# Optimization experiments

Measured on AMD Instinct MI355X. Metric: run time of the kernel, lower is better.

Reference implementation:

```python
import jax, jax.numpy as jnp
import numpy as np

N, D = 50000, 1000
FH1, FH2 = 256, 128
GH1, GH2, H = 64, 30, 3
NC = 10
E = 800000
BN_EPS = 1e-5


def setup_inputs() -> dict:
    key = jax.random.key(0)
    ks = iter(jax.random.split(key, 48))
    nk = lambda: next(ks)
    r = lambda *s: jax.random.normal(nk(), s, jnp.float32) * 0.05
    g = lambda n: 1.0 + jax.random.normal(nk(), (n,), jnp.float32) * 0.01
    return dict(
        x=jax.random.normal(nk(), (N, D), jnp.float32),
        edge_index=jax.random.randint(nk(), (2, E), 0, N, dtype=jnp.int32),
        enc_w1=r(D, FH1), enc_b1=r(FH1), enc_g1=g(FH1), enc_bt1=r(FH1),
        enc_w2=r(FH1, FH2), enc_b2=r(FH2), enc_g2=g(FH2), enc_bt2=r(FH2),
        gat1_w=r(FH2, H * GH1), gat1_asrc=r(H, GH1), gat1_adst=r(H, GH1), gat1_b=r(H * GH1),
        gat2_w=r(H * GH1, GH2), gat2_asrc=r(1, GH2), gat2_adst=r(1, GH2), gat2_b=r(GH2),
        gat3_w=r(H * GH1, GH2), gat3_asrc=r(1, GH2), gat3_adst=r(1, GH2), gat3_b=r(GH2),
        dec_w1=r(GH2, FH2), dec_b1=r(FH2), dec_g1=g(FH2), dec_bt1=r(FH2),
        dec_w2=r(FH2, FH1), dec_b2=r(FH1), dec_g2=g(FH1), dec_bt2=r(FH1),
        dec_w3=r(FH1, D), dec_b3=r(D),
        clu_w1=r(GH2, FH2), clu_b1=r(FH2), clu_g1=g(FH2), clu_bt1=r(FH2),
        clu_w2=r(FH2, NC), clu_b2=r(NC),
    )


def _bn_elu(h, w, b, gm, bt):
    # Linear -> BatchNorm1d (batch stats) -> ELU; dropout is identity at eval
    h = h @ w + b
    m = h.mean(0)
    v = h.var(0)
    return jax.nn.elu(gm * (h - m) * jax.lax.rsqrt(v + BN_EPS) + bt)


def _gat(h, src, dst, n, w, a_src, a_dst, b, heads, oc, concat):
    # PyG GATConv: per-head linear, edge-wise LeakyReLU(0.2) scores,
    # softmax over incoming edges of each dst node, weighted scatter-sum.
    hh = (h @ w).reshape(n, heads, oc)            # [N,H,C]
    s_src = jnp.sum(hh * a_src, -1)               # [N,H]
    s_dst = jnp.sum(hh * a_dst, -1)               # [N,H]
    e = jax.nn.leaky_relu(s_src[src] + s_dst[dst], negative_slope=0.2)  # [E,H]
    m = jax.ops.segment_max(e, dst, num_segments=n)
    p = jnp.exp(e - m[dst])
    denom = jax.ops.segment_sum(p, dst, num_segments=n)
    alpha = p / denom[dst]                        # [E,H]
    msg = hh[src] * alpha[..., None]              # [E,H,C]
    out = jax.ops.segment_sum(msg, dst, num_segments=n)
    out = out.reshape(n, heads * oc) if concat else out.mean(1)
    return out + b


def reference(x, edge_index,
              enc_w1, enc_b1, enc_g1, enc_bt1, enc_w2, enc_b2, enc_g2, enc_bt2,
              gat1_w, gat1_asrc, gat1_adst, gat1_b,
              gat2_w, gat2_asrc, gat2_adst, gat2_b,
              gat3_w, gat3_asrc, gat3_adst, gat3_b,
              dec_w1, dec_b1, dec_g1, dec_bt1, dec_w2, dec_b2, dec_g2, dec_bt2, dec_w3, dec_b3,
              clu_w1, clu_b1, clu_g1, clu_bt1, clu_w2, clu_b2):
    n = x.shape[0]
    loops = jnp.arange(n, dtype=edge_index.dtype)  # GATConv add_self_loops=True
    src = jnp.concatenate([edge_index[0], loops])
    dst = jnp.concatenate([edge_index[1], loops])

    h = _bn_elu(x, enc_w1, enc_b1, enc_g1, enc_bt1)
    h = _bn_elu(h, enc_w2, enc_b2, enc_g2, enc_bt2)
    h = jax.nn.relu(_gat(h, src, dst, n, gat1_w, gat1_asrc, gat1_adst, gat1_b, H, GH1, True))
    mu = _gat(h, src, dst, n, gat2_w, gat2_asrc, gat2_adst, gat2_b, 1, GH2, False)
    logvar = _gat(h, src, dst, n, gat3_w, gat3_asrc, gat3_adst, gat3_b, 1, GH2, False)
    z = mu  # eval-mode reparameterize returns mu

    d = _bn_elu(z, dec_w1, dec_b1, dec_g1, dec_bt1)
    d = _bn_elu(d, dec_w2, dec_b2, dec_g2, dec_bt2)
    x_rec = d @ dec_w3 + dec_b3

    c = _bn_elu(z, clu_w1, clu_b1, clu_g1, clu_bt1)
    pred = jax.nn.softmax(c @ clu_w2 + clu_b2, axis=1)
    return (pred, x_rec, z, mu, logvar)
```

## Files before the change

### kernel.cpp

```cpp
#include <hip/hip_runtime.h>
#include <hip/hip_bf16.h>

typedef short short8 __attribute__((ext_vector_type(8)));
typedef short short4v __attribute__((ext_vector_type(4)));
typedef float f32x4 __attribute__((ext_vector_type(4)));

static __device__ __forceinline__ short f2bf(float f){
  __hip_bfloat16 h = __float2bfloat16(f);
  return __builtin_bit_cast(short, h);
}
static __device__ __forceinline__ float b2f(short s){
  unsigned int u = ((unsigned int)(unsigned short)s) << 16;
  return __builtin_bit_cast(float, u);
}
static __device__ __forceinline__ float lrelu(float x){ return x > 0.f ? x : 0.2f*x; }
static __device__ __forceinline__ float eluf(float x){ return x > 0.f ? x : (__expf(x)-1.f); }
static __device__ __forceinline__ int imin(int a,int b){ return a<b?a:b; }

typedef const __attribute__((address_space(1))) void as1_void;
typedef __attribute__((address_space(3))) void as3_void;
static __device__ __forceinline__ void gload16(const void* g, void* l){
  __builtin_amdgcn_global_load_lds((as1_void*)g, (as3_void*)l, 16, 0, 0);
}
template<int NN> __device__ __forceinline__ void wait_vm(){
  if constexpr (NN==0) asm volatile("s_waitcnt vmcnt(0)" ::: "memory");
  else if constexpr (NN==3) asm volatile("s_waitcnt vmcnt(3)" ::: "memory");
  else if constexpr (NN==4) asm volatile("s_waitcnt vmcnt(4)" ::: "memory");
  else if constexpr (NN==6) asm volatile("s_waitcnt vmcnt(6)" ::: "memory");
  else if constexpr (NN==8) asm volatile("s_waitcnt vmcnt(8)" ::: "memory");
}

__global__ __launch_bounds__(256) void cvt_x(const float* __restrict__ x, short* __restrict__ xb, int M){
  int row = blockIdx.x*2 + (threadIdx.x>>7);
  int c8  = (threadIdx.x&127)*8;
  if (row >= M || c8 >= 1000) return;
  const float* p = x + (size_t)row*1000 + c8;
  float4 f0 = *(const float4*)p, f1 = *(const float4*)(p+4);
  short8 o;
  o[0]=f2bf(f0.x);o[1]=f2bf(f0.y);o[2]=f2bf(f0.z);o[3]=f2bf(f0.w);
  o[4]=f2bf(f1.x);o[5]=f2bf(f1.y);o[6]=f2bf(f1.z);o[7]=f2bf(f1.w);
  *(short8*)&xb[(size_t)row*1000 + c8] = o;
}

template<int BN, bool OBF16, bool CSTATS>
__global__ __launch_bounds__(256) void gemm_g(
    const short* __restrict__ A, int lda, const short* __restrict__ Bt, int ldb,
    void* __restrict__ Cv, const float* __restrict__ bias,
    float* __restrict__ ssum, float* __restrict__ ssq,
    int M, int N, int K, int ldc)
{
  constexpr int BM = 128, BK = 32, GPR = 4;
  constexpr int WN = BN/2, FM = 4, FN = WN/16;
  constexpr int AI = (BM*GPR)/(4*64);
  constexpr int BI_T = (BN*GPR)/64;
  constexpr bool BDUP = (BI_T < 4);
  constexpr int BI = BDUP ? BI_T : BI_T/4;
  constexpr int LPT = AI + BI;
  constexpr int TS = (BM+BN)*BK;
  __shared__ short lds[4][TS];

  const int tid = threadIdx.x, wid = tid>>6, lane = tid&63;
  const int wm = wid>>1, wn = wid&1;
  const int bm = blockIdx.x*BM, bn = blockIdx.y*BN;
  const int lr = lane&15, lg = lane>>4;
  const int nt = (K + BK - 1)/BK;

  f32x4 acc[FM][FN] = {};

  auto STAGE = [&](int t){
    int buf = t & 3, k0 = t*BK;
    #pragma unroll
    for (int i=0;i<AI;i++){
      int ci = wid*AI + i;
      int c = ci*64 + lane;
      int row = c>>2, g = c&3;
      int gr = imin(bm+row, M-1);
      const short* src = A + (size_t)gr*lda + k0 + ((g ^ (row&3))<<3);
      gload16(src, &lds[buf][ci*512]);
    }
    #pragma unroll
    for (int i=0;i<BI;i++){
      int bi = BDUP ? i : wid*BI + i;
      int c = bi*64 + lane;
      int row = c>>2, g = c&3;
      const short* src = Bt + (size_t)(bn+row)*ldb + k0 + ((g ^ (row&3))<<3);
      gload16(src, &lds[buf][BM*BK + bi*512]);
    }
  };

  for (int s=0; s<3 && s<nt; ++s) STAGE(s);

  for (int t=0; t<nt; ++t){
    int newer = imin(nt, t+3) - t - 1;
    if (newer >= 2) wait_vm<2*LPT>();
    else if (newer == 1) wait_vm<LPT>();
    else wait_vm<0>();
    __builtin_amdgcn_s_barrier();
    __builtin_amdgcn_sched_barrier(0);
    if (t+3 < nt) STAGE(t+3);
    int buf = t & 3;
    short8 af[FM], bf[FN];
    #pragma unroll
    for (int m=0;m<FM;m++){
      int r = wm*64 + m*16 + lr;
      af[m] = *(short8*)&lds[buf][r*BK + ((lg ^ (r&3))<<3)];
    }
    #pragma unroll
    for (int n=0;n<FN;n++){
      int r = wn*WN + n*16 + lr;
      bf[n] = *(short8*)&lds[buf][BM*BK + r*BK + ((lg ^ (r&3))<<3)];
    }
    #pragma unroll
    for (int m=0;m<FM;m++)
      #pragma unroll
      for (int n=0;n<FN;n++)
        acc[m][n] = __builtin_amdgcn_mfma_f32_16x16x32_bf16(af[m], bf[n], acc[m][n], 0, 0, 0);
  }

  #pragma unroll
  for (int m=0;m<FM;m++)
    #pragma unroll
    for (int n=0;n<FN;n++)
      #pragma unroll
      for (int q=0;q<4;q++){
        int row = bm + wm*64 + m*16 + lg*4 + q;
        int col = bn + wn*WN + n*16 + lr;
        if (row < M && col < N){
          float v = acc[m][n][q];
          if (bias) v += bias[col];
          if (OBF16) ((short*)Cv)[(size_t)row*ldc + col] = f2bf(v);
          else       ((float*)Cv)[(size_t)row*ldc + col] = v;
        }
      }
  if (CSTATS){
    #pragma unroll
    for (int n=0;n<FN;n++){
      float s = 0.f, q2 = 0.f;
      #pragma unroll
      for (int m=0;m<FM;m++)
        #pragma unroll
        for (int q=0;q<4;q++){
          int row = bm + wm*64 + m*16 + lg*4 + q;
          if (row < M){ float v = acc[m][n][q]; s += v; q2 += v*v; }
        }
      s  += __shfl_xor(s, 16);  s += __shfl_xor(s, 32);
      q2 += __shfl_xor(q2, 16); q2 += __shfl_xor(q2, 32);
      if (lg == 0){
        int col = bn + wn*WN + n*16 + lr;
        atomicAdd(&ssum[col], s);
        atomicAdd(&ssq[col],  q2);
      }
    }
  }
}

struct WEnt { const float* src; short* dst; int K, N, KP, NR; };
struct WTab { WEnt e[10]; };
__global__ __launch_bounds__(256) void wtrans_all(WTab tab){
  WEnt w = tab.e[blockIdx.y];
  int gid = blockIdx.x*256 + threadIdx.x;
  if (gid >= w.NR * w.KP) return;
  int n = gid / w.KP, k = gid - n*w.KP;
  float v = (k < w.K && n < w.N) ? w.src[(size_t)k*w.N + n] : 0.f;
  w.dst[gid] = f2bf(v);
}

template<int C>
__global__ __launch_bounds__(256) void bn_elu_apply2(const float* __restrict__ H, short* __restrict__ O,
    int M, float invM,
    const float* __restrict__ ssum, const float* __restrict__ ssq,
    const float* __restrict__ g, const float* __restrict__ bt){
  __shared__ float sc[C], sh[C];
  for (int c = threadIdx.x; c < C; c += 256){
    float mn  = ssum[c]*invM;
    float var = ssq[c]*invM - mn*mn;
    float s = g[c]*rsqrtf(var + 1e-5f);
    sc[c] = s; sh[c] = bt[c] - mn*s;
  }
  __syncthreads();
  int total4 = M*(C/4);
  for (int i = blockIdx.x*256+threadIdx.x; i < total4; i += gridDim.x*256){
    float4 v = ((const float4*)H)[i];
    int cb = (i*4) & (C-1);
    short4v o;
    o[0] = f2bf(eluf(v.x*sc[cb+0]+sh[cb+0]));
    o[1] = f2bf(eluf(v.y*sc[cb+1]+sh[cb+1]));
    o[2] = f2bf(eluf(v.z*sc[cb+2]+sh[cb+2]));
    o[3] = f2bf(eluf(v.w*sc[cb+3]+sh[cb+3]));
    ((short4v*)O)[i] = o;
  }
}

__global__ __launch_bounds__(256) void bn_elu_split(const float* __restrict__ H,
    short* __restrict__ Od, short* __restrict__ Oc, int M, float invM,
    const float* __restrict__ ssum, const float* __restrict__ ssq,
    const float* __restrict__ gd, const float* __restrict__ btd,
    const float* __restrict__ gc, const float* __restrict__ btc){
  __shared__ float sc[256], sh[256];
  {
    int c = threadIdx.x;
    float mn  = ssum[c]*invM;
    float var = ssq[c]*invM - mn*mn;
    float gg = (c<128) ? gd[c] : gc[c-128];
    float bb = (c<128) ? btd[c] : btc[c-128];
    float s = gg*rsqrtf(var + 1e-5f);
    sc[c] = s; sh[c] = bb - mn*s;
  }
  __syncthreads();
  int total4 = M*64;
  for (int i = blockIdx.x*256+threadIdx.x; i < total4; i += gridDim.x*256){
    float4 v = ((const float4*)H)[i];
    int cb = (i*4) & 255;
    short4v o;
    o[0] = f2bf(eluf(v.x*sc[cb+0]+sh[cb+0]));
    o[1] = f2bf(eluf(v.y*sc[cb+1]+sh[cb+1]));
    o[2] = f2bf(eluf(v.z*sc[cb+2]+sh[cb+2]));
    o[3] = f2bf(eluf(v.w*sc[cb+3]+sh[cb+3]));
    int row = i>>6;
    short* O = (cb < 128) ? Od : Oc;
    *(short4v*)&O[(size_t)row*128 + (cb&127)] = o;
  }
}

__global__ void hist_kernel(const int* __restrict__ d, int E, int* __restrict__ deg){
  int i = blockIdx.x*256 + threadIdx.x;
  if (i < E) atomicAdd(&deg[d[i]], 1);
}
__global__ __launch_bounds__(256) void scan1(const int* __restrict__ deg, int* __restrict__ offs,
                                             int* __restrict__ bsum, int n){
  __shared__ int sm[256];
  int tid = threadIdx.x;
  int base = blockIdx.x*1024 + tid*4;
  int v0 = base+0<n ? deg[base+0] : 0;
  int v1 = base+1<n ? deg[base+1] : 0;
  int v2 = base+2<n ? deg[base+2] : 0;
  int v3 = base+3<n ? deg[base+3] : 0;
  int ts = v0+v1+v2+v3;
  sm[tid] = ts;
  __syncthreads();
  #pragma unroll
  for (int d=1; d<256; d<<=1){
    int t = (tid>=d) ? sm[tid-d] : 0;
    __syncthreads();
    sm[tid] += t;
    __syncthreads();
  }
  int ex = sm[tid] - ts;
  if (base+0<n) offs[base+0] = ex;
  if (base+1<n) offs[base+1] = ex+v0;
  if (base+2<n) offs[base+2] = ex+v0+v1;
  if (base+3<n) offs[base+3] = ex+v0+v1+v2;
  if (tid==255) bsum[blockIdx.x] = sm[255];
}
__global__ __launch_bounds__(256) void scan3(int* __restrict__ offs, const int* __restrict__ bsum,
                      int* __restrict__ cursor, int n, int total){
  __shared__ int base_sm;
  int tgt = blockIdx.x >> 2;
  if (threadIdx.x < 64){
    int j = threadIdx.x;
    int v = (j < tgt) ? bsum[j] : 0;
    #pragma unroll
    for (int d=32; d; d>>=1) v += __shfl_xor(v, d);
    if (j == 0) base_sm = v;
  }
  __syncthreads();
  int i = blockIdx.x*256 + threadIdx.x;
  if (i < n){ int v = offs[i] + base_sm; offs[i]=v; cursor[i]=v; }
  if (i == 0) offs[n] = total;
}
__global__ void scatter_kernel(const int* __restrict__ s, const int* __restrict__ d, int E,
                               int* __restrict__ cursor, int* __restrict__ csr){
  int i = blockIdx.x*256 + threadIdx.x;
  if (i < E){ int pos = atomicAdd(&cursor[d[i]], 1); csr[pos] = s[i]; }
}

__global__ __launch_bounds__(256) void gat1_scores_bf(const short* __restrict__ hh,
    const float* __restrict__ as, const float* __restrict__ ad,
    float* __restrict__ ss, float* __restrict__ sd, int n){
  int w = threadIdx.x >> 6, lane = threadIdx.x & 63;
  int row = blockIdx.x*4 + w;
  if (row >= n) return;
  const short* hr = hh + (size_t)row*192;
  float ps[3], pd[3];
  #pragma unroll
  for (int h=0; h<3; h++){
    float v = b2f(hr[h*64 + lane]);
    ps[h] = v * as[h*64+lane];
    pd[h] = v * ad[h*64+lane];
  }
  #pragma unroll
  for (int m=32; m; m>>=1){
    #pragma unroll
    for (int h=0;h<3;h++){ ps[h] += __shfl_xor(ps[h], m); pd[h] += __shfl_xor(pd[h], m); }
  }
  if (lane == 0){
    #pragma unroll
    for (int h=0;h<3;h++){ ss[row*3+h]=ps[h]; sd[row*3+h]=pd[h]; }
  }
}

__global__ __launch_bounds__(256) void gat1_gather_bf(const int* __restrict__ offs, const int* __restrict__ csr,
    const short* __restrict__ hh, const float* __restrict__ ss, const float* __restrict__ sd,
    const float* __restrict__ bias, short* __restrict__ out, int n){
  int w = threadIdx.x >> 6, lane = threadIdx.x & 63;
  int dst = blockIdx.x*4 + w;
  if (dst >= n) return;
  float sd0 = sd[dst*3+0], sd1 = sd[dst*3+1], sd2 = sd[dst*3+2];
  float p0 = __expf(lrelu(ss[dst*3+0]+sd0));
  float p1 = __expf(lrelu(ss[dst*3+1]+sd1));
  float p2 = __expf(lrelu(ss[dst*3+2]+sd2));
  const short* hr = hh + (size_t)dst*192;
  float a0 = p0*b2f(hr[lane]), a1 = p1*b2f(hr[64+lane]), a2 = p2*b2f(hr[128+lane]);
  float d0 = p0, d1 = p1, d2 = p2;
  int p = offs[dst], pe = offs[dst+1];
  for (; p+4 <= pe; p += 4){
    int s0=csr[p], s1=csr[p+1], s2=csr[p+2], s3=csr[p+3];
    float e00=ss[s0*3+0], e01=ss[s0*3+1], e02=ss[s0*3+2];
    float e10=ss[s1*3+0], e11=ss[s1*3+1], e12=ss[s1*3+2];
    float e20=ss[s2*3+0], e21=ss[s2*3+1], e22=ss[s2*3+2];
    float e30=ss[s3*3+0], e31=ss[s3*3+1], e32=ss[s3*3+2];
    const short* r0 = hh + (size_t)s0*192;
    const short* r1 = hh + (size_t)s1*192;
    const short* r2 = hh + (size_t)s2*192;
    const short* r3 = hh + (size_t)s3*192;
    float v00=b2f(r0[lane]), v01=b2f(r0[64+lane]), v02=b2f(r0[128+lane]);
    float v10=b2f(r1[lane]), v11=b2f(r1[64+lane]), v12=b2f(r1[128+lane]);
    float v20=b2f(r2[lane]), v21=b2f(r2[64+lane]), v22=b2f(r2[128+lane]);
    float v30=b2f(r3[lane]), v31=b2f(r3[64+lane]), v32=b2f(r3[128+lane]);
    float q00=__expf(lrelu(e00+sd0)), q01=__expf(lrelu(e01+sd1)), q02=__expf(lrelu(e02+sd2));
    float q10=__expf(lrelu(e10+sd0)), q11=__expf(lrelu(e11+sd1)), q12=__expf(lrelu(e12+sd2));
    float q20=__expf(lrelu(e20+sd0)), q21=__expf(lrelu(e21+sd1)), q22=__expf(lrelu(e22+sd2));
    float q30=__expf(lrelu(e30+sd0)), q31=__expf(lrelu(e31+sd1)), q32=__expf(lrelu(e32+sd2));
    a0 += q00*v00 + q10*v10 + q20*v20 + q30*v30;
    a1 += q01*v01 + q11*v11 + q21*v21 + q31*v31;
    a2 += q02*v02 + q12*v12 + q22*v22 + q32*v32;
    d0 += q00+q10+q20+q30;
    d1 += q01+q11+q21+q31;
    d2 += q02+q12+q22+q32;
  }
  for (; p < pe; ++p){
    int src = csr[p];
    float q0 = __expf(lrelu(ss[src*3+0]+sd0));
    float q1 = __expf(lrelu(ss[src*3+1]+sd1));
    float q2 = __expf(lrelu(ss[src*3+2]+sd2));
    const short* sr = hh + (size_t)src*192;
    a0 += q0*b2f(sr[lane]); a1 += q1*b2f(sr[64+lane]); a2 += q2*b2f(sr[128+lane]);
    d0 += q0; d1 += q1; d2 += q2;
  }
  float v0 = a0/d0 + bias[lane];
  float v1 = a1/d1 + bias[64+lane];
  float v2 = a2/d2 + bias[128+lane];
  short* orow = out + (size_t)dst*192;
  orow[lane]      = f2bf(v0 > 0.f ? v0 : 0.f);
  orow[64+lane]   = f2bf(v1 > 0.f ? v1 : 0.f);
  orow[128+lane]  = f2bf(v2 > 0.f ? v2 : 0.f);
}

__global__ __launch_bounds__(256) void gat23_scores(const float* __restrict__ hh23,
    const float* __restrict__ a2s, const float* __restrict__ a2d,
    const float* __restrict__ a3s, const float* __restrict__ a3d,
    float* __restrict__ s2s, float* __restrict__ s2d, float* __restrict__ s3s, float* __restrict__ s3d, int n){
  int w = threadIdx.x >> 6, lane = threadIdx.x & 63;
  int row = blockIdx.x*4 + w;
  if (row >= n) return;
  float p[4] = {0.f,0.f,0.f,0.f};
  if (lane < 30){
    float v2 = hh23[(size_t)row*64+lane], v3 = hh23[(size_t)row*64+32+lane];
    p[0]=v2*a2s[lane]; p[1]=v2*a2d[lane]; p[2]=v3*a3s[lane]; p[3]=v3*a3d[lane];
  }
  #pragma unroll
  for (int m=32; m; m>>=1){
    #pragma unroll
    for (int j=0;j<4;j++) p[j] += __shfl_xor(p[j], m);
  }
  if (lane == 0){ s2s[row]=p[0]; s2d[row]=p[1]; s3s[row]=p[2]; s3d[row]=p[3]; }
}

__global__ __launch_bounds__(256) void gat23_gather(const int* __restrict__ offs, const int* __restrict__ csr,
    const float* __restrict__ hh23,
    const float* __restrict__ s2s, const float* __restrict__ s2d,
    const float* __restrict__ s3s, const float* __restrict__ s3d,
    const float* __restrict__ b2, const float* __restrict__ b3,
    float* __restrict__ zs, float* __restrict__ mus, float* __restrict__ lvs,
    short* __restrict__ zbf, int n){
  int w = threadIdx.x >> 6, lane = threadIdx.x & 63;
  int dst = blockIdx.x*4 + w;
  if (dst >= n) return;
  bool lo = lane < 32;
  int c = lane & 31;
  bool valid = c < 30;
  float sdA = s2d[dst], sdB = s3d[dst];
  float sdx = lo ? sdA : sdB;
  const float* ssx = lo ? s2s : s3s;
  float p2 = __expf(lrelu(s2s[dst]+sdA));
  float p3 = __expf(lrelu(s3s[dst]+sdB));
  float val = valid ? hh23[(size_t)dst*64+lane] : 0.f;
  float acc = (lo ? p2 : p3) * val;
  float den2 = p2, den3 = p3;
  int p = offs[dst], pe = offs[dst+1];
  for (; p+4 <= pe; p += 4){
    int s0=csr[p], s1=csr[p+1], s2i=csr[p+2], s3i=csr[p+3];
    float eA0=ssx[s0], eA1=ssx[s1], eA2=ssx[s2i], eA3=ssx[s3i];
    float f20=s2s[s0], f21=s2s[s1], f22=s2s[s2i], f23=s2s[s3i];
    float f30=s3s[s0], f31=s3s[s1], f32=s3s[s2i], f33=s3s[s3i];
    float v0 = valid ? hh23[(size_t)s0*64+lane] : 0.f;
    float v1 = valid ? hh23[(size_t)s1*64+lane] : 0.f;
    float v2 = valid ? hh23[(size_t)s2i*64+lane] : 0.f;
    float v3 = valid ? hh23[(size_t)s3i*64+lane] : 0.f;
    float qx0=__expf(lrelu(eA0+sdx)), qx1=__expf(lrelu(eA1+sdx));
    float qx2=__expf(lrelu(eA2+sdx)), qx3=__expf(lrelu(eA3+sdx));
    acc += qx0*v0 + qx1*v1 + qx2*v2 + qx3*v3;
    den2 += __expf(lrelu(f20+sdA)) + __expf(lrelu(f21+sdA)) + __expf(lrelu(f22+sdA)) + __expf(lrelu(f23+sdA));
    den3 += __expf(lrelu(f30+sdB)) + __expf(lrelu(f31+sdB)) + __expf(lrelu(f32+sdB)) + __expf(lrelu(f33+sdB));
  }
  for (; p < pe; ++p){
    int src = csr[p];
    float q2 = __expf(lrelu(s2s[src]+sdA));
    float q3 = __expf(lrelu(s3s[src]+sdB));
    float v = valid ? hh23[(size_t)src*64+lane] : 0.f;
    acc += (lo ? q2 : q3) * v;
    den2 += q2; den3 += q3;
  }
  if (lo){
    if (valid){
      float v = acc/den2 + b2[c];
      zs[(size_t)dst*30+c]  = v;
      mus[(size_t)dst*30+c] = v;
      zbf[(size_t)dst*32+c] = f2bf(v);
    } else {
      zbf[(size_t)dst*32+c] = 0;
    }
  } else if (valid){
    lvs[(size_t)dst*30+c] = acc/den3 + b3[c];
  }
}

__global__ __launch_bounds__(256) void softmax10(const float* __restrict__ in, float* __restrict__ out, int n){
  int row = blockIdx.x*256 + threadIdx.x;
  if (row >= n) return;
  const float* r = in + (size_t)row*10;
  float m = r[0];
  #pragma unroll
  for (int j=1;j<10;j++) m = fmaxf(m, r[j]);
  float e[10], s = 0.f;
  #pragma unroll
  for (int j=0;j<10;j++){ e[j] = __expf(r[j]-m); s += e[j]; }
  float inv = 1.f/s;
  float* o = out + (size_t)row*10;
  #pragma unroll
  for (int j=0;j<10;j++) o[j] = e[j]*inv;
}

static inline int cdiv(int a, int b){ return (a + b - 1) / b; }

extern "C" void kernel_launch(void* const* d_in, const int* in_sizes, int n_in,
                              void* d_out, int out_size, void* d_ws, size_t ws_size,
                              hipStream_t stream)
{
  const float* x        = (const float*)d_in[0];
  const int*   ei       = (const int*)  d_in[1];
  const float* enc_w1   = (const float*)d_in[2];
  const float* enc_g1   = (const float*)d_in[4];
  const float* enc_bt1  = (const float*)d_in[5];
  const float* enc_w2   = (const float*)d_in[6];
  const float* enc_g2   = (const float*)d_in[8];
  const float* enc_bt2  = (const float*)d_in[9];
  const float* gat1_w   = (const float*)d_in[10];
  const float* gat1_as  = (const float*)d_in[11];
  const float* gat1_ad  = (const float*)d_in[12];
  const float* gat1_b   = (const float*)d_in[13];
  const float* gat2_w   = (const float*)d_in[14];
  const float* gat2_as  = (const float*)d_in[15];
  const float* gat2_ad  = (const float*)d_in[16];
  const float* gat2_b   = (const float*)d_in[17];
  const float* gat3_w   = (const float*)d_in[18];
  const float* gat3_as  = (const float*)d_in[19];
  const float* gat3_ad  = (const float*)d_in[20];
  const float* gat3_b   = (const float*)d_in[21];
  const float* dec_w1   = (const float*)d_in[22];
  const float* dec_g1   = (const float*)d_in[24];
  const float* dec_bt1  = (const float*)d_in[25];
  const float* dec_w2   = (const float*)d_in[26];
  const float* dec_g2   = (const float*)d_in[28];
  const float* dec_bt2  = (const float*)d_in[29];
  const float* dec_w3   = (const float*)d_in[30];
  const float* dec_b3   = (const float*)d_in[31];
  const float* clu_w1   = (const float*)d_in[32];
  const float* clu_g1   = (const float*)d_in[34];
  const float* clu_bt1  = (const float*)d_in[35];
  const float* clu_w2   = (const float*)d_in[36];
  const float* clu_b2   = (const float*)d_in[37];

  const int N = in_sizes[0] / 1000;
  const int E = in_sizes[1] / 2;
  const int* e_src = ei;
  const int* e_dst = ei + E;
  const float invN = 1.f/(float)N;

  float* out  = (float*)d_out;
  float* pred = out;
  float* xrec = out + (size_t)N*10;
  float* zs   = xrec + (size_t)N*1000;
  float* mus  = zs  + (size_t)N*30;
  float* lvs  = mus + (size_t)N*30;

  char* ws = (char*)d_ws;
  size_t off = 0;
  auto alloc = [&](size_t bytes)->char*{
    char* p = ws + off;
    off = (off + bytes + 255) & ~(size_t)255;
    return p;
  };
  short* t_enc1  = (short*)alloc(256*1024*2);
  short* t_enc2  = (short*)alloc(128*256*2);
  short* t_gat1  = (short*)alloc(192*128*2);
  short* t_gat23 = (short*)alloc(64*192*2);
  short* t_dc1   = (short*)alloc(256*32*2);
  short* t_dec2  = (short*)alloc(256*128*2);
  short* t_dec3  = (short*)alloc(1024*256*2);
  short* t_clu2  = (short*)alloc(32*128*2);
  float* h1f  = (float*)alloc((size_t)N*256*4);
  short* h1b  = (short*)alloc((size_t)N*256*2);
  float* h2f  = (float*)alloc((size_t)N*128*4);
  short* h2b  = (short*)alloc((size_t)N*128*2);
  short* hh1b = (short*)alloc((size_t)N*192*2);
  short* h3b  = (short*)alloc((size_t)N*192*2);
  float* hh23f= (float*)alloc((size_t)N*64*4);
  short* zbf  = (short*)alloc((size_t)N*32*2);
  float* ss1  = (float*)alloc((size_t)N*3*4);
  float* sd1  = (float*)alloc((size_t)N*3*4);
  float* s2s  = (float*)alloc((size_t)N*4);
  float* s2d  = (float*)alloc((size_t)N*4);
  float* s3s  = (float*)alloc((size_t)N*4);
  float* s3d  = (float*)alloc((size_t)N*4);
  float* stats= (float*)alloc(2048*4);
  int*   deg  = (int*)alloc((size_t)(N+1)*4);
  int*   offs = (int*)alloc((size_t)(N+1)*4);
  int*   curp = (int*)alloc((size_t)(N+1)*4);
  int*   bsum = (int*)alloc(256*4);
  int*   csr  = (int*)alloc((size_t)E*4);
  short* xb   = h1b;
  float* dc1f = h2f;
  short* d1b  = h3b;
  short* c1b  = (short*)hh23f;
  float* d2f  = h1f;
  short* d2b  = h1b;
  float* c2   = (float*)zbf;
  float* st_enc1 = stats, *st_enc2 = stats+512, *st_dc1 = stats+768, *st_dec2 = stats+1280;

  WTab tab;
  tab.e[0] = {enc_w1, t_enc1, 1000, 256, 1024, 256};
  tab.e[1] = {enc_w2, t_enc2, 256, 128, 256, 128};
  tab.e[2] = {gat1_w, t_gat1, 128, 192, 128, 192};
  tab.e[3] = {gat2_w, t_gat23, 192, 30, 192, 32};
  tab.e[4] = {gat3_w, t_gat23 + 32*192, 192, 30, 192, 32};
  tab.e[5] = {dec_w1, t_dc1, 30, 128, 32, 128};
  tab.e[6] = {clu_w1, t_dc1 + 128*32, 30, 128, 32, 128};
  tab.e[7] = {dec_w2, t_dec2, 128, 256, 128, 256};
  tab.e[8] = {dec_w3, t_dec3, 256, 1000, 256, 1024};
  tab.e[9] = {clu_w2, t_clu2, 128, 10, 128, 32};
  wtrans_all<<<dim3(1024, 10), 256, 0, stream>>>(tab);
  hipMemsetAsync(stats, 0, 2048*4, stream);
  hipMemsetAsync(deg, 0, (size_t)(N+1)*4, stream);

  hist_kernel<<<cdiv(E,256), 256, 0, stream>>>(e_dst, E, deg);
  int nb = cdiv(N, 1024);
  scan1<<<nb, 256, 0, stream>>>(deg, offs, bsum, N);
  scan3<<<cdiv(N,256), 256, 0, stream>>>(offs, bsum, curp, N, E);
  scatter_kernel<<<cdiv(E,256), 256, 0, stream>>>(e_src, e_dst, E, curp, csr);

  const int MB = cdiv(N, 128);

  cvt_x<<<cdiv(N,2), 256, 0, stream>>>(x, xb, N);
  gemm_g<128,false,true><<<dim3(MB,2), 256, 0, stream>>>(xb, 1000, t_enc1, 1024, h1f, nullptr, st_enc1, st_enc1+256, N, 256, 1000, 256);
  bn_elu_apply2<256><<<2048, 256, 0, stream>>>(h1f, h1b, N, invN, st_enc1, st_enc1+256, enc_g1, enc_bt1);

  gemm_g<128,false,true><<<dim3(MB,1), 256, 0, stream>>>(h1b, 256, t_enc2, 256, h2f, nullptr, st_enc2, st_enc2+128, N, 128, 256, 128);
  bn_elu_apply2<128><<<2048, 256, 0, stream>>>(h2f, h2b, N, invN, st_enc2, st_enc2+128, enc_g2, enc_bt2);

  gemm_g<64,true,false><<<dim3(MB,3), 256, 0, stream>>>(h2b, 128, t_gat1, 128, hh1b, nullptr, nullptr, nullptr, N, 192, 128, 192);
  gat1_scores_bf<<<cdiv(N,4), 256, 0, stream>>>(hh1b, gat1_as, gat1_ad, ss1, sd1, N);
  gat1_gather_bf<<<cdiv(N,4), 256, 0, stream>>>(offs, csr, hh1b, ss1, sd1, gat1_b, h3b, N);

  gemm_g<64,false,false><<<dim3(MB,1), 256, 0, stream>>>(h3b, 192, t_gat23, 192, hh23f, nullptr, nullptr, nullptr, N, 64, 192, 64);
  gat23_scores<<<cdiv(N,4), 256, 0, stream>>>(hh23f, gat2_as, gat2_ad, gat3_as, gat3_ad, s2s, s2d, s3s, s3d, N);
  gat23_gather<<<cdiv(N,4), 256, 0, stream>>>(offs, csr, hh23f, s2s, s2d, s3s, s3d, gat2_b, gat3_b, zs, mus, lvs, zbf, N);

  gemm_g<128,false,true><<<dim3(MB,2), 256, 0, stream>>>(zbf, 32, t_dc1, 32, dc1f, nullptr, st_dc1, st_dc1+256, N, 256, 32, 256);
  bn_elu_split<<<2048, 256, 0, stream>>>(dc1f, d1b, c1b, N, invN, st_dc1, st_dc1+256, dec_g1, dec_bt1, clu_g1, clu_bt1);

  gemm_g<128,false,true><<<dim3(MB,2), 256, 0, stream>>>(d1b, 128, t_dec2, 128, d2f, nullptr, st_dec2, st_dec2+256, N, 256, 128, 256);
  bn_elu_apply2<256><<<2048, 256, 0, stream>>>(d2f, d2b, N, invN, st_dec2, st_dec2+256, dec_g2, dec_bt2);

  gemm_g<128,false,false><<<dim3(MB,8), 256, 0, stream>>>(d2b, 256, t_dec3, 256, xrec, dec_b3, nullptr, nullptr, N, 1000, 256, 1000);

  gemm_g<32,false,false><<<dim3(MB,1), 256, 0, stream>>>(c1b, 128, t_clu2, 128, c2, clu_b2, nullptr, nullptr, N, 10, 128, 10);
  softmax10<<<cdiv(N,256), 256, 0, stream>>>(c2, pred, N);
}
```

Baseline: 701.5 us.

## Fuse fp32 conversion and BatchNorm-ELU into GEMM A-operand loading

Replaces the GEMM with a 64x128-tile, 512-thread kernel that reads fp32 activations straight from global memory, applies the BatchNorm scale/shift and ELU per column while converting to bf16, and writes the result into LDS. This removes the separate x conversion kernel and all bn_elu_apply/split passes along with their bf16 intermediate buffers. It also software-prefetches CSR indices in both GAT gather loops. The cost is that A is now loaded through registers instead of direct global-to-LDS loads, and each column tile recomputes the activation, with padded weight tables added to cover the new tile shapes.

```diff
diff --git a/kernel.cpp b/kernel.cpp
--- a/kernel.cpp
+++ b/kernel.cpp
@@ -24,138 +24,153 @@
 }
 template<int NN> __device__ __forceinline__ void wait_vm(){
   if constexpr (NN==0) asm volatile("s_waitcnt vmcnt(0)" ::: "memory");
+  else if constexpr (NN==1) asm volatile("s_waitcnt vmcnt(1)" ::: "memory");
   else if constexpr (NN==3) asm volatile("s_waitcnt vmcnt(3)" ::: "memory");
-  else if constexpr (NN==4) asm volatile("s_waitcnt vmcnt(4)" ::: "memory");
-  else if constexpr (NN==6) asm volatile("s_waitcnt vmcnt(6)" ::: "memory");
-  else if constexpr (NN==8) asm volatile("s_waitcnt vmcnt(8)" ::: "memory");
-}
-
-__global__ __launch_bounds__(256) void cvt_x(const float* __restrict__ x, short* __restrict__ xb, int M){
-  int row = blockIdx.x*2 + (threadIdx.x>>7);
-  int c8  = (threadIdx.x&127)*8;
-  if (row >= M || c8 >= 1000) return;
-  const float* p = x + (size_t)row*1000 + c8;
-  float4 f0 = *(const float4*)p, f1 = *(const float4*)(p+4);
-  short8 o;
-  o[0]=f2bf(f0.x);o[1]=f2bf(f0.y);o[2]=f2bf(f0.z);o[3]=f2bf(f0.w);
-  o[4]=f2bf(f1.x);o[5]=f2bf(f1.y);o[6]=f2bf(f1.z);o[7]=f2bf(f1.w);
-  *(short8*)&xb[(size_t)row*1000 + c8] = o;
-}
-
-template<int BN, bool OBF16, bool CSTATS>
-__global__ __launch_bounds__(256) void gemm_g(
-    const short* __restrict__ A, int lda, const short* __restrict__ Bt, int ldb,
-    void* __restrict__ Cv, const float* __restrict__ bias,
-    float* __restrict__ ssum, float* __restrict__ ssq,
-    int M, int N, int K, int ldc)
+  else if constexpr (NN==5) asm volatile("s_waitcnt vmcnt(5)" ::: "memory");
+}
+
+template<bool AF32, bool AFF, bool OBF16, bool CST>
+__global__ __launch_bounds__(512, 4) void gemm_r(
+    const void* __restrict__ Av, int lda, const short* __restrict__ Bt, int ldb,
+    void* __restrict__ Cv, int ldc, const float* __restrict__ bias,
+    int M, int N, int K,
+    const float* __restrict__ a_sum, const float* __restrict__ a_sq,
+    const float* __restrict__ a_g, const float* __restrict__ a_bt, float invM,
+    float* __restrict__ o_sum, float* __restrict__ o_sq)
 {
-  constexpr int BM = 128, BK = 32, GPR = 4;
-  constexpr int WN = BN/2, FM = 4, FN = WN/16;
-  constexpr int AI = (BM*GPR)/(4*64);
-  constexpr int BI_T = (BN*GPR)/64;
-  constexpr bool BDUP = (BI_T < 4);
-  constexpr int BI = BDUP ? BI_T : BI_T/4;
-  constexpr int LPT = AI + BI;
-  constexpr int TS = (BM+BN)*BK;
-  __shared__ short lds[4][TS];
+  constexpr int BM=64, BN=128, BK=32;
+  __shared__ short Asm[4][BM*BK];
+  __shared__ short Bsm[4][BN*BK];
+  __shared__ float s_sc[256], s_sh[256];
 
   const int tid = threadIdx.x, wid = tid>>6, lane = tid&63;
   const int wm = wid>>1, wn = wid&1;
   const int bm = blockIdx.x*BM, bn = blockIdx.y*BN;
   const int lr = lane&15, lg = lane>>4;
   const int nt = (K + BK - 1)/BK;
-
-  f32x4 acc[FM][FN] = {};
-
-  auto STAGE = [&](int t){
-    int buf = t & 3, k0 = t*BK;
+  const float* A32 = (const float*)Av;
+  const short* A16 = (const short*)Av;
+
+  const int arow = tid>>3, ag = tid&7;
+  const int agr  = imin(bm + arow, M-1);
+  const int awr  = arow*BK + (((ag>>1) ^ (arow&3))<<3) + (ag&1)*4;
+  const int brow = tid>>2, bg = tid&3;
+  const short* bptr = Bt + (size_t)(bn+brow)*ldb + ((bg ^ (brow&3))<<3);
+
+  f32x4 acc[4] = {};
+  float4  raf[4];
+  short4v ras[4];
+
+  #define ISSUE(T, S) do{                                                     \
+    if ((T) < nt){                                                            \
+      int k_ = (T)*BK + ag*4;                                                 \
+      if (AF32){ int kk_ = imin(k_, K-4);                                     \
+        raf[S] = *(const float4*)(A32 + (size_t)agr*lda + kk_); }             \
+      else { ras[S] = *(const short4v*)(A16 + (size_t)agr*lda + k_); }        \
+      gload16(bptr + (size_t)(T)*BK, (void*)&Bsm[S][wid*512]);                \
+    } }while(0)
+
+  #define WRA(T, S) do{                                                       \
+    if ((T) < nt){                                                            \
+      short4v o_;                                                             \
+      if (AF32){                                                              \
+        float4 f_ = raf[S];                                                   \
+        if (AFF){ int k0_ = (T)*BK + ag*4;                                    \
+          float4 sc_ = *(const float4*)&s_sc[k0_];                            \
+          float4 sh_ = *(const float4*)&s_sh[k0_];                            \
+          f_.x = eluf(f_.x*sc_.x+sh_.x); f_.y = eluf(f_.y*sc_.y+sh_.y);       \
+          f_.z = eluf(f_.z*sc_.z+sh_.z); f_.w = eluf(f_.w*sc_.w+sh_.w); }     \
+        o_[0]=f2bf(f_.x); o_[1]=f2bf(f_.y); o_[2]=f2bf(f_.z); o_[3]=f2bf(f_.w);\
+      } else { o_ = ras[S]; }                                                 \
+      *(short4v*)&Asm[S][awr] = o_;                                           \
+    } }while(0)
+
+  #define BODY(T, S, SW, SI) do{                                              \
+    if ((T) < nt){                                                            \
+      if ((T)+2 < nt) wait_vm<3>(); else if ((T)+1 < nt) wait_vm<1>();        \
+      else wait_vm<0>();                                                      \
+      WRA((T)+1, SW);                                                         \
+      asm volatile("s_waitcnt lgkmcnt(0)" ::: "memory");                      \
+      __builtin_amdgcn_sched_barrier(0);                                      \
+      __builtin_amdgcn_s_barrier();                                           \
+      __builtin_amdgcn_sched_barrier(0);                                      \
+      int ra_ = wm*16 + lr;                                                   \
+      short8 af_ = *(short8*)&Asm[S][ra_*BK + ((lg ^ (ra_&3))<<3)];           \
+      short8 bf_[4];                                                          \
+      _Pragma("unroll")                                                       \
+      for (int n_=0;n_<4;n_++){ int rb_ = wn*64 + n_*16 + lr;                 \
+        bf_[n_] = *(short8*)&Bsm[S][rb_*BK + ((lg ^ (rb_&3))<<3)]; }          \
+      ISSUE((T)+3, SI);                                                       \
+      _Pragma("unroll")                                                       \
+      for (int n_=0;n_<4;n_++)                                                \
+        acc[n_] = __builtin_amdgcn_mfma_f32_16x16x32_bf16(af_, bf_[n_], acc[n_], 0,0,0); \
+    } }while(0)
+
+  ISSUE(0,0); ISSUE(1,1); ISSUE(2,2);
+  if (AFF){
+    for (int k = tid; k < K; k += 512){
+      float mn = a_sum[k]*invM;
+      float vr = a_sq[k]*invM - mn*mn;
+      float s  = a_g[k]*rsqrtf(vr + 1e-5f);
+      s_sc[k] = s; s_sh[k] = a_bt[k] - mn*s;
+    }
+    asm volatile("s_waitcnt lgkmcnt(0)" ::: "memory");
+    __builtin_amdgcn_sched_barrier(0);
+    __builtin_amdgcn_s_barrier();
+  }
+  if (nt >= 3) wait_vm<5>(); else if (nt == 2) wait_vm<3>(); else wait_vm<1>();
+  WRA(0, 0);
+  asm volatile("s_waitcnt lgkmcnt(0)" ::: "memory");
+  __builtin_amdgcn_sched_barrier(0);
+  __builtin_amdgcn_s_barrier();
+  __builtin_amdgcn_sched_barrier(0);
+
+  for (int t = 0; t < nt; t += 4){
+    BODY(t+0, 0, 1, 3);
+    BODY(t+1, 1, 2, 0);
+    BODY(t+2, 2, 3, 1);
+    BODY(t+3, 3, 0, 2);
+  }
+  #undef ISSUE
+  #undef WRA
+  #undef BODY
+
+  const int rowb = bm + wm*16 + lg*4;
+  #pragma unroll
+  for (int n=0;n<4;n++){
+    int col = bn + wn*64 + n*16 + lr;
     #pragma unroll
-    for (int i=0;i<AI;i++){
-      int ci = wid*AI + i;
-      int c = ci*64 + lane;
-      int row = c>>2, g = c&3;
-      int gr = imin(bm+row, M-1);
-      const short* src = A + (size_t)gr*lda + k0 + ((g ^ (row&3))<<3);
-      gload16(src, &lds[buf][ci*512]);
+    for (int q=0;q<4;q++){
+      int row = rowb + q;
+      if (row < M && col < N){
+        float v = acc[n][q];
+        if (bias) v += bias[col];
+        if (OBF16) ((short*)Cv)[(size_t)row*ldc + col] = f2bf(v);
+        else       ((float*)Cv)[(size_t)row*ldc + col] = v;
+      }
     }
+  }
+  if (CST){
     #pragma unroll
-    for (int i=0;i<BI;i++){
-      int bi = BDUP ? i : wid*BI + i;
-      int c = bi*64 + lane;
-      int row = c>>2, g = c&3;
-      const short* src = Bt + (size_t)(bn+row)*ldb + k0 + ((g ^ (row&3))<<3);
-      gload16(src, &lds[buf][BM*BK + bi*512]);
-    }
-  };
-
-  for (int s=0; s<3 && s<nt; ++s) STAGE(s);
-
-  for (int t=0; t<nt; ++t){
-    int newer = imin(nt, t+3) - t - 1;
-    if (newer >= 2) wait_vm<2*LPT>();
-    else if (newer == 1) wait_vm<LPT>();
-    else wait_vm<0>();
-    __builtin_amdgcn_s_barrier();
-    __builtin_amdgcn_sched_barrier(0);
-    if (t+3 < nt) STAGE(t+3);
-    int buf = t & 3;
-    short8 af[FM], bf[FN];
-    #pragma unroll
-    for (int m=0;m<FM;m++){
-      int r = wm*64 + m*16 + lr;
-      af[m] = *(short8*)&lds[buf][r*BK + ((lg ^ (r&3))<<3)];
-    }
-    #pragma unroll
-    for (int n=0;n<FN;n++){
-      int r = wn*WN + n*16 + lr;
-      bf[n] = *(short8*)&lds[buf][BM*BK + r*BK + ((lg ^ (r&3))<<3)];
-    }
-    #pragma unroll
-    for (int m=0;m<FM;m++)
-      #pragma unroll
-      for (int n=0;n<FN;n++)
-        acc[m][n] = __builtin_amdgcn_mfma_f32_16x16x32_bf16(af[m], bf[n], acc[m][n], 0, 0, 0);
-  }
-
-  #pragma unroll
-  for (int m=0;m<FM;m++)
-    #pragma unroll
-    for (int n=0;n<FN;n++)
+    for (int n=0;n<4;n++){
+      float s = 0.f, q2 = 0.f;
       #pragma unroll
       for (int q=0;q<4;q++){
-        int row = bm + wm*64 + m*16 + lg*4 + q;
-        int col = bn + wn*WN + n*16 + lr;
-        if (row < M && col < N){
-          float v = acc[m][n][q];
-          if (bias) v += bias[col];
-          if (OBF16) ((short*)Cv)[(size_t)row*ldc + col] = f2bf(v);
-          else       ((float*)Cv)[(size_t)row*ldc + col] = v;
-        }
+        int row = rowb + q;
+        if (row < M){ float v = acc[n][q]; s += v; q2 += v*v; }
       }
-  if (CSTATS){
-    #pragma unroll
-    for (int n=0;n<FN;n++){
-      float s = 0.f, q2 = 0.f;
-      #pragma unroll
-      for (int m=0;m<FM;m++)
-        #pragma unroll
-        for (int q=0;q<4;q++){
-          int row = bm + wm*64 + m*16 + lg*4 + q;
-          if (row < M){ float v = acc[m][n][q]; s += v; q2 += v*v; }
-        }
       s  += __shfl_xor(s, 16);  s += __shfl_xor(s, 32);
       q2 += __shfl_xor(q2, 16); q2 += __shfl_xor(q2, 32);
       if (lg == 0){
-        int col = bn + wn*WN + n*16 + lr;
-        atomicAdd(&ssum[col], s);
-        atomicAdd(&ssq[col],  q2);
+        int col = bn + wn*64 + n*16 + lr;
+        if (col < N){ atomicAdd(&o_sum[col], s); atomicAdd(&o_sq[col], q2); }
       }
     }
   }
 }
 
 struct WEnt { const float* src; short* dst; int K, N, KP, NR; };
-struct WTab { WEnt e[10]; };
+struct WTab { WEnt e[12]; };
 __global__ __launch_bounds__(256) void wtrans_all(WTab tab){
   WEnt w = tab.e[blockIdx.y];
   int gid = blockIdx.x*256 + threadIdx.x;
@@ -163,63 +178,6 @@
   int n = gid / w.KP, k = gid - n*w.KP;
   float v = (k < w.K && n < w.N) ? w.src[(size_t)k*w.N + n] : 0.f;
   w.dst[gid] = f2bf(v);
-}
-
-template<int C>
-__global__ __launch_bounds__(256) void bn_elu_apply2(const float* __restrict__ H, short* __restrict__ O,
-    int M, float invM,
-    const float* __restrict__ ssum, const float* __restrict__ ssq,
-    const float* __restrict__ g, const float* __restrict__ bt){
-  __shared__ float sc[C], sh[C];
-  for (int c = threadIdx.x; c < C; c += 256){
-    float mn  = ssum[c]*invM;
-    float var = ssq[c]*invM - mn*mn;
-    float s = g[c]*rsqrtf(var + 1e-5f);
-    sc[c] = s; sh[c] = bt[c] - mn*s;
-  }
-  __syncthreads();
-  int total4 = M*(C/4);
-  for (int i = blockIdx.x*256+threadIdx.x; i < total4; i += gridDim.x*256){
-    float4 v = ((const float4*)H)[i];
-    int cb = (i*4) & (C-1);
-    short4v o;
-    o[0] = f2bf(eluf(v.x*sc[cb+0]+sh[cb+0]));
-    o[1] = f2bf(eluf(v.y*sc[cb+1]+sh[cb+1]));
-    o[2] = f2bf(eluf(v.z*sc[cb+2]+sh[cb+2]));
-    o[3] = f2bf(eluf(v.w*sc[cb+3]+sh[cb+3]));
-    ((short4v*)O)[i] = o;
-  }
-}
-
-__global__ __launch_bounds__(256) void bn_elu_split(const float* __restrict__ H,
-    short* __restrict__ Od, short* __restrict__ Oc, int M, float invM,
-    const float* __restrict__ ssum, const float* __restrict__ ssq,
-    const float* __restrict__ gd, const float* __restrict__ btd,
-    const float* __restrict__ gc, const float* __restrict__ btc){
-  __shared__ float sc[256], sh[256];
-  {
-    int c = threadIdx.x;
-    float mn  = ssum[c]*invM;
-    float var = ssq[c]*invM - mn*mn;
-    float gg = (c<128) ? gd[c] : gc[c-128];
-    float bb = (c<128) ? btd[c] : btc[c-128];
-    float s = gg*rsqrtf(var + 1e-5f);
-    sc[c] = s; sh[c] = bb - mn*s;
-  }
-  __syncthreads();
-  int total4 = M*64;
-  for (int i = blockIdx.x*256+threadIdx.x; i < total4; i += gridDim.x*256){
-    float4 v = ((const float4*)H)[i];
-    int cb = (i*4) & 255;
-    short4v o;
-    o[0] = f2bf(eluf(v.x*sc[cb+0]+sh[cb+0]));
-    o[1] = f2bf(eluf(v.y*sc[cb+1]+sh[cb+1]));
-    o[2] = f2bf(eluf(v.z*sc[cb+2]+sh[cb+2]));
-    o[3] = f2bf(eluf(v.w*sc[cb+3]+sh[cb+3]));
-    int row = i>>6;
-    short* O = (cb < 128) ? Od : Oc;
-    *(short4v*)&O[(size_t)row*128 + (cb&127)] = o;
-  }
 }
 
 __global__ void hist_kernel(const int* __restrict__ d, int E, int* __restrict__ deg){
@@ -313,8 +271,12 @@
   float a0 = p0*b2f(hr[lane]), a1 = p1*b2f(hr[64+lane]), a2 = p2*b2f(hr[128+lane]);
   float d0 = p0, d1 = p1, d2 = p2;
   int p = offs[dst], pe = offs[dst+1];
-  for (; p+4 <= pe; p += 4){
-    int s0=csr[p], s1=csr[p+1], s2=csr[p+2], s3=csr[p+3];
+  int n0=0,n1=0,n2=0,n3=0;
+  if (p+4 <= pe){ n0=csr[p]; n1=csr[p+1]; n2=csr[p+2]; n3=csr[p+3]; }
+  while (p+4 <= pe){
+    int s0=n0, s1=n1, s2=n2, s3=n3;
+    int pn = p+4;
+    if (pn+4 <= pe){ n0=csr[pn]; n1=csr[pn+1]; n2=csr[pn+2]; n3=csr[pn+3]; }
     float e00=ss[s0*3+0], e01=ss[s0*3+1], e02=ss[s0*3+2];
     float e10=ss[s1*3+0], e11=ss[s1*3+1], e12=ss[s1*3+2];
     float e20=ss[s2*3+0], e21=ss[s2*3+1], e22=ss[s2*3+2];
@@ -337,6 +299,7 @@
     d0 += q00+q10+q20+q30;
     d1 += q01+q11+q21+q31;
     d2 += q02+q12+q22+q32;
+    p = pn;
   }
   for (; p < pe; ++p){
     int src = csr[p];
@@ -398,8 +361,12 @@
   float acc = (lo ? p2 : p3) * val;
   float den2 = p2, den3 = p3;
   int p = offs[dst], pe = offs[dst+1];
-  for (; p+4 <= pe; p += 4){
-    int s0=csr[p], s1=csr[p+1], s2i=csr[p+2], s3i=csr[p+3];
+  int n0=0,n1=0,n2=0,n3=0;
+  if (p+4 <= pe){ n0=csr[p]; n1=csr[p+1]; n2=csr[p+2]; n3=csr[p+3]; }
+  while (p+4 <= pe){
+    int s0=n0, s1=n1, s2i=n2, s3i=n3;
+    int pn = p+4;
+    if (pn+4 <= pe){ n0=csr[pn]; n1=csr[pn+1]; n2=csr[pn+2]; n3=csr[pn+3]; }
     float eA0=ssx[s0], eA1=ssx[s1], eA2=ssx[s2i], eA3=ssx[s3i];
     float f20=s2s[s0], f21=s2s[s1], f22=s2s[s2i], f23=s2s[s3i];
     float f30=s3s[s0], f31=s3s[s1], f32=s3s[s2i], f33=s3s[s3i];
@@ -412,6 +379,7 @@
     acc += qx0*v0 + qx1*v1 + qx2*v2 + qx3*v3;
     den2 += __expf(lrelu(f20+sdA)) + __expf(lrelu(f21+sdA)) + __expf(lrelu(f22+sdA)) + __expf(lrelu(f23+sdA));
     den3 += __expf(lrelu(f30+sdB)) + __expf(lrelu(f31+sdB)) + __expf(lrelu(f32+sdB)) + __expf(lrelu(f33+sdB));
+    p = pn;
   }
   for (; p < pe; ++p){
     int src = csr[p];
@@ -513,53 +481,49 @@
   };
   short* t_enc1  = (short*)alloc(256*1024*2);
   short* t_enc2  = (short*)alloc(128*256*2);
-  short* t_gat1  = (short*)alloc(192*128*2);
-  short* t_gat23 = (short*)alloc(64*192*2);
+  short* t_gat1  = (short*)alloc(256*128*2);
+  short* t_gat23 = (short*)alloc(128*192*2);
   short* t_dc1   = (short*)alloc(256*32*2);
   short* t_dec2  = (short*)alloc(256*128*2);
   short* t_dec3  = (short*)alloc(1024*256*2);
-  short* t_clu2  = (short*)alloc(32*128*2);
-  float* h1f  = (float*)alloc((size_t)N*256*4);
-  short* h1b  = (short*)alloc((size_t)N*256*2);
-  float* h2f  = (float*)alloc((size_t)N*128*4);
-  short* h2b  = (short*)alloc((size_t)N*128*2);
-  short* hh1b = (short*)alloc((size_t)N*192*2);
-  short* h3b  = (short*)alloc((size_t)N*192*2);
-  float* hh23f= (float*)alloc((size_t)N*64*4);
-  short* zbf  = (short*)alloc((size_t)N*32*2);
-  float* ss1  = (float*)alloc((size_t)N*3*4);
-  float* sd1  = (float*)alloc((size_t)N*3*4);
-  float* s2s  = (float*)alloc((size_t)N*4);
-  float* s2d  = (float*)alloc((size_t)N*4);
-  float* s3s  = (float*)alloc((size_t)N*4);
-  float* s3d  = (float*)alloc((size_t)N*4);
-  float* stats= (float*)alloc(2048*4);
-  int*   deg  = (int*)alloc((size_t)(N+1)*4);
-  int*   offs = (int*)alloc((size_t)(N+1)*4);
-  int*   curp = (int*)alloc((size_t)(N+1)*4);
-  int*   bsum = (int*)alloc(256*4);
-  int*   csr  = (int*)alloc((size_t)E*4);
-  short* xb   = h1b;
-  float* dc1f = h2f;
-  short* d1b  = h3b;
-  short* c1b  = (short*)hh23f;
-  float* d2f  = h1f;
-  short* d2b  = h1b;
+  short* t_clu2  = (short*)alloc(128*128*2);
+  float* h1f   = (float*)alloc((size_t)N*256*4);
+  float* h2f   = (float*)alloc((size_t)N*128*4);
+  short* hh1b  = (short*)alloc((size_t)N*192*2);
+  short* h3b   = (short*)alloc((size_t)N*192*2);
+  float* hh23f = (float*)alloc((size_t)N*64*4);
+  short* zbf   = (short*)alloc((size_t)N*32*2);
+  float* ss1   = (float*)alloc((size_t)N*3*4);
+  float* sd1   = (float*)alloc((size_t)N*3*4);
+  float* s2s   = (float*)alloc((size_t)N*4);
+  float* s2d   = (float*)alloc((size_t)N*4);
+  float* s3s   = (float*)alloc((size_t)N*4);
+  float* s3d   = (float*)alloc((size_t)N*4);
+  float* stats = (float*)alloc(2048*4);
+  int*   deg   = (int*)alloc((size_t)(N+1)*4);
+  int*   offs  = (int*)alloc((size_t)(N+1)*4);
+  int*   curp  = (int*)alloc((size_t)(N+1)*4);
+  int*   bsum  = (int*)alloc(256*4);
+  int*   csr   = (int*)alloc((size_t)E*4);
+  float* dc1f = h1f;
+  float* d2f  = h2f;
   float* c2   = (float*)zbf;
-  float* st_enc1 = stats, *st_enc2 = stats+512, *st_dc1 = stats+768, *st_dec2 = stats+1280;
+  float* st_enc1 = stats, *st_enc2 = stats+512, *st_dc1 = stats+1024, *st_dec2 = stats+1536;
 
   WTab tab;
-  tab.e[0] = {enc_w1, t_enc1, 1000, 256, 1024, 256};
-  tab.e[1] = {enc_w2, t_enc2, 256, 128, 256, 128};
-  tab.e[2] = {gat1_w, t_gat1, 128, 192, 128, 192};
-  tab.e[3] = {gat2_w, t_gat23, 192, 30, 192, 32};
-  tab.e[4] = {gat3_w, t_gat23 + 32*192, 192, 30, 192, 32};
-  tab.e[5] = {dec_w1, t_dc1, 30, 128, 32, 128};
-  tab.e[6] = {clu_w1, t_dc1 + 128*32, 30, 128, 32, 128};
-  tab.e[7] = {dec_w2, t_dec2, 128, 256, 128, 256};
-  tab.e[8] = {dec_w3, t_dec3, 256, 1000, 256, 1024};
-  tab.e[9] = {clu_w2, t_clu2, 128, 10, 128, 32};
-  wtrans_all<<<dim3(1024, 10), 256, 0, stream>>>(tab);
+  tab.e[0]  = {enc_w1, t_enc1, 1000, 256, 1024, 256};
+  tab.e[1]  = {enc_w2, t_enc2, 256, 128, 256, 128};
+  tab.e[2]  = {gat1_w, t_gat1, 128, 192, 128, 256};
+  tab.e[3]  = {gat2_w, t_gat23, 192, 30, 192, 32};
+  tab.e[4]  = {gat3_w, t_gat23 + 32*192, 192, 30, 192, 32};
+  tab.e[5]  = {gat2_w, t_gat23 + 64*192, 192, 0, 192, 64};
+  tab.e[6]  = {dec_w1, t_dc1, 30, 128, 32, 128};
+  tab.e[7]  = {clu_w1, t_dc1 + 128*32, 30, 128, 32, 128};
+  tab.e[8]  = {dec_w2, t_dec2, 128, 256, 128, 256};
+  tab.e[9]  = {dec_w3, t_dec3, 256, 1000, 256, 1024};
+  tab.e[10] = {clu_w2, t_clu2, 128, 10, 128, 128};
+  tab.e[11] = {enc_w1, t_enc1, 0, 0, 0, 0};
+  wtrans_all<<<dim3(1024, 12), 256, 0, stream>>>(tab);
   hipMemsetAsync(stats, 0, 2048*4, stream);
   hipMemsetAsync(deg, 0, (size_t)(N+1)*4, stream);
 
@@ -569,31 +533,37 @@
   scan3<<<cdiv(N,256), 256, 0, stream>>>(offs, bsum, curp, N, E);
   scatter_kernel<<<cdiv(E,256), 256, 0, stream>>>(e_src, e_dst, E, curp, csr);
 
-  const int MB = cdiv(N, 128);
-
-  cvt_x<<<cdiv(N,2), 256, 0, stream>>>(x, xb, N);
-  gemm_g<128,false,true><<<dim3(MB,2), 256, 0, stream>>>(xb, 1000, t_enc1, 1024, h1f, nullptr, st_enc1, st_enc1+256, N, 256, 1000, 256);
-  bn_elu_apply2<256><<<2048, 256, 0, stream>>>(h1f, h1b, N, invN, st_enc1, st_enc1+256, enc_g1, enc_bt1);
-
-  gemm_g<128,false,true><<<dim3(MB,1), 256, 0, stream>>>(h1b, 256, t_enc2, 256, h2f, nullptr, st_enc2, st_enc2+128, N, 128, 256, 128);
-  bn_elu_apply2<128><<<2048, 256, 0, stream>>>(h2f, h2b, N, invN, st_enc2, st_enc2+128, enc_g2, enc_bt2);
-
-  gemm_g<64,true,false><<<dim3(MB,3), 256, 0, stream>>>(h2b, 128, t_gat1, 128, hh1b, nullptr, nullptr, nullptr, N, 192, 128, 192);
+  const int MB = cdiv(N, 64);
+
+  gemm_r<true,false,false,true><<<dim3(MB,2), 512, 0, stream>>>(
+      x, 1000, t_enc1, 1024, h1f, 256, nullptr, N, 256, 1000,
+      nullptr, nullptr, nullptr, nullptr, 0.f, st_enc1, st_enc1+256);
+  gemm_r<true,true,false,true><<<dim3(MB,1), 512, 0, stream>>>(
+      h1f, 256, t_enc2, 256, h2f, 128, nullptr, N, 128, 256,
+      st_enc1, st_enc1+256, enc_g1, enc_bt1, invN, st_enc2, st_enc2+256);
+  gemm_r<true,true,true,false><<<dim3(MB,2), 512, 0, stream>>>(
+      h2f, 128, t_gat1, 128, hh1b, 192, nullptr, N, 192, 128,
+      st_enc2, st_enc2+256, enc_g2, enc_bt2, invN, nullptr, nullptr);
   gat1_scores_bf<<<cdiv(N,4), 256, 0, stream>>>(hh1b, gat1_as, gat1_ad, ss1, sd1, N);
   gat1_gather_bf<<<cdiv(N,4), 256, 0, stream>>>(offs, csr, hh1b, ss1, sd1, gat1_b, h3b, N);
 
-  gemm_g<64,false,false><<<dim3(MB,1), 256, 0, stream>>>(h3b, 192, t_gat23, 192, hh23f, nullptr, nullptr, nullptr, N, 64, 192, 64);
+  gemm_r<false,false,false,false><<<dim3(MB,1), 512, 0, stream>>>(
+      h3b, 192, t_gat23, 192, hh23f, 64, nullptr, N, 64, 192,
+      nullptr, nullptr, nullptr, nullptr, 0.f, nullptr, nullptr);
   gat23_scores<<<cdiv(N,4), 256, 0, stream>>>(hh23f, gat2_as, gat2_ad, gat3_as, gat3_ad, s2s, s2d, s3s, s3d, N);
   gat23_gather<<<cdiv(N,4), 256, 0, stream>>>(offs, csr, hh23f, s2s, s2d, s3s, s3d, gat2_b, gat3_b, zs, mus, lvs, zbf, N);
 
-  gemm_g<128,false,true><<<dim3(MB,2), 256, 0, stream>>>(zbf, 32, t_dc1, 32, dc1f, nullptr, st_dc1, st_dc1+256, N, 256, 32, 256);
-  bn_elu_split<<<2048, 256, 0, stream>>>(dc1f, d1b, c1b, N, invN, st_dc1, st_dc1+256, dec_g1, dec_bt1, clu_g1, clu_bt1);
-
-  gemm_g<128,false,true><<<dim3(MB,2), 256, 0, stream>>>(d1b, 128, t_dec2, 128, d2f, nullptr, st_dec2, st_dec2+256, N, 256, 128, 256);
-  bn_elu_apply2<256><<<2048, 256, 0, stream>>>(d2f, d2b, N, invN, st_dec2, st_dec2+256, dec_g2, dec_bt2);
-
-  gemm_g<128,false,false><<<dim3(MB,8), 256, 0, stream>>>(d2b, 256, t_dec3, 256, xrec, dec_b3, nullptr, nullptr, N, 1000, 256, 1000);
-
-  gemm_g<32,false,false><<<dim3(MB,1), 256, 0, stream>>>(c1b, 128, t_clu2, 128, c2, clu_b2, nullptr, nullptr, N, 10, 128, 10);
+  gemm_r<false,false,false,true><<<dim3(MB,2), 512, 0, stream>>>(
+      zbf, 32, t_dc1, 32, dc1f, 256, nullptr, N, 256, 32,
+      nullptr, nullptr, nullptr, nullptr, 0.f, st_dc1, st_dc1+256);
+  gemm_r<true,true,false,true><<<dim3(MB,2), 512, 0, stream>>>(
+      dc1f, 256, t_dec2, 128, d2f, 256, nullptr, N, 256, 128,
+      st_dc1, st_dc1+256, dec_g1, dec_bt1, invN, st_dec2, st_dec2+256);
+  gemm_r<true,true,false,false><<<dim3(MB,8), 512, 0, stream>>>(
+      d2f, 256, t_dec3, 256, xrec, 1000, dec_b3, N, 1000, 256,
+      st_dec2, st_dec2+256, dec_g2, dec_bt2, invN, nullptr, nullptr);
+  gemm_r<true,true,false,false><<<dim3(MB,1), 512, 0, stream>>>(
+      dc1f + 128, 256, t_clu2, 128, c2, 10, clu_b2, N, 10, 128,
+      st_dc1+128, st_dc1+256+128, clu_g1, clu_bt1, invN, nullptr, nullptr);
   softmax10<<<cdiv(N,256), 256, 0, stream>>>(c2, pred, N);
 }
```

Result: slower. 981.7 us (+40.0%).
